# Kernel optimization log

Measured on AMD Instinct MI355X. Metric: run time of the kernel, lower is better.

The kernel has to match this reference:

```python
import jax, jax.numpy as jnp
import numpy as np

# ----- static configuration (mirrors __init__) -----
NUM_CLASSES = np.array([2, 4, 8, 16, 32] * 8, dtype=np.int64)   # 40 categorical features
F_FEAT = len(NUM_CLASSES)                                        # 40
D = int(NUM_CLASSES.sum())                                       # 496 one-hot columns
T = 1000                                                         # num diffusion timesteps
B = 32768                                                        # batch size

OFFSETS_NP = np.concatenate([[0], np.cumsum(NUM_CLASSES)])
SEG_IDS = jnp.asarray(np.repeat(np.arange(F_FEAT), NUM_CLASSES))                    # [D] col -> feature
NC_EXPANDED = jnp.asarray(np.repeat(NUM_CLASSES, NUM_CLASSES).astype(np.float32))   # [D]
LOG_NC = jnp.log(NC_EXPANDED)
SEG_START = jnp.asarray(OFFSETS_NP[:-1])                                            # [F] segment start col

_beta = np.linspace(1e-4, 0.02, T)
_alpha = 1.0 - _beta
_ca = np.cumprod(_alpha)
LOG_ALPHA = jnp.asarray(np.log(_alpha), jnp.float32)
LOG_1M_ALPHA = jnp.asarray(np.log(1.0 - _alpha), jnp.float32)
LOG_CA = jnp.asarray(np.log(_ca), jnp.float32)
LOG_1M_CA = jnp.asarray(np.log(1.0 - _ca), jnp.float32)


def _extract(a, t):
    return a[t][:, None]  # [B,1]


def seg_logsumexp(x):
    """Per-categorical-segment stable logsumexp of x [B,D], broadcast back to [B,D]."""
    xt = x.T                                                       # [D,B]
    m = jax.ops.segment_max(xt, SEG_IDS, num_segments=F_FEAT)      # [F,B]
    mg = m[SEG_IDS]                                                # [D,B]
    s = jax.ops.segment_sum(jnp.exp(xt - mg), SEG_IDS, num_segments=F_FEAT)
    return (m + jnp.log(s))[SEG_IDS].T                             # [B,D]


def index_to_log_onehot(x):
    """x [B,F] per-feature class indices -> log one-hot [B,D] (log(clamp(onehot,1e-30)))."""
    cols = SEG_START[None, :] + x                                  # global cols [B,F]
    oh = jnp.zeros((x.shape[0], D), jnp.float32)
    oh = oh.at[jnp.arange(x.shape[0])[:, None], cols].set(1.0)
    return jnp.log(jnp.maximum(oh, 1e-30))


def q_prior(log_x0, t):
    return jnp.logaddexp(log_x0 + _extract(LOG_CA, t), _extract(LOG_1M_CA, t) - LOG_NC[None, :])


def q_one_timestep(log_xt, t):
    return jnp.logaddexp(log_xt + _extract(LOG_ALPHA, t), _extract(LOG_1M_ALPHA, t) - LOG_NC[None, :])


def q_posterior(log_x0, log_xt, t):
    tm1 = jnp.maximum(t - 1, 0)
    ev = q_prior(log_x0, tm1)
    ev = jnp.where((t == 0)[:, None], log_x0, ev)
    un = ev + q_one_timestep(log_xt, t)
    return un - seg_logsumexp(un)


def log_sample_categorical(logits, uniform):
    """Gumbel-max sample per ragged segment; returns log one-hot [B,D]."""
    gumbel = -jnp.log(-jnp.log(uniform + 1e-30) + 1e-30)
    z = gumbel + logits                                            # [B,D]
    zt = z.T                                                       # [D,B]
    m = jax.ops.segment_max(zt, SEG_IDS, num_segments=F_FEAT)[SEG_IDS]   # [D,B]
    cand = jnp.where(zt == m, jnp.arange(D)[:, None], D)           # first-max tie break (= torch argmax)
    col = jax.ops.segment_min(cand, SEG_IDS, num_segments=F_FEAT).T      # [B,F] winning global column
    oh = jnp.zeros(z.shape, jnp.float32).at[jnp.arange(z.shape[0])[:, None], col].set(1.0)
    return jnp.log(jnp.maximum(oh, 1e-30))


def setup_inputs():
    key = jax.random.key(0)
    k1, k2, k3, k4, k5 = jax.random.split(key, 5)
    x_0 = jax.random.randint(k1, (B, F_FEAT), 0, jnp.asarray(NUM_CLASSES)[None, :]).astype(jnp.int32)
    timesteps = jax.random.randint(k2, (B,), 0, T).astype(jnp.int32)
    uniform = jax.random.uniform(k3, (B, D), jnp.float32)
    W = jax.random.normal(k4, (D, D), jnp.float32) * 0.02
    b = jnp.zeros((D,), jnp.float32)
    t_emb = jax.random.normal(k5, (T, D), jnp.float32) * 0.02
    return {"x_0": x_0, "timesteps": timesteps, "uniform": uniform, "W": W, "b": b, "t_emb": t_emb}


def reference(x_0, timesteps, uniform, W, b, t_emb):
    log_x0 = index_to_log_onehot(x_0)                              # [B,D]
    log_xt = log_sample_categorical(q_prior(log_x0, timesteps), uniform)   # multinomial_q_sample
    pred = log_xt @ W + b + t_emb[timesteps]                       # denoise_fn(log_x_t, t)
    log_x0_hat = pred - seg_logsumexp(pred)                        # per-class log_softmax
    log_true = q_posterior(log_x0, log_xt, timesteps)
    log_est = q_posterior(log_x0_hat, log_xt, timesteps)
    kl = jnp.sum(jnp.exp(log_true) * (log_true - log_est), axis=1)         # [B]
    dec_nll = -jnp.sum(jnp.exp(log_x0) * log_est, axis=1)                  # [B]
    mask = (timesteps == 0).astype(jnp.float32)
    diff_loss = mask * dec_nll + (1.0 - mask) * kl
    log_qxT = q_prior(log_x0, jnp.full((log_x0.shape[0],), T - 1, jnp.int32))
    kl_prior = jnp.sum(jnp.exp(log_qxT) * (log_qxT + LOG_NC[None, :]), axis=1)  # vs log_half = -log(K)
    loss = diff_loss * T + kl_prior
    return jnp.mean(loss)
```

## Files before the change

### kernel.cpp

```cpp
#include <hip/hip_runtime.h>
#include <math.h>

#define NFEAT 40
#define NCOLS 496
#define NT    1000
#define NB    32768
#define LC    (-69.07755278982137f)

#define LK2  0.6931471805599453f
#define LK4  1.3862943611198906f
#define LK8  2.0794415416798357f
#define LK16 2.772588722239781f
#define LK32 3.4657359027997265f

#define WS_TABS   0
#define WS_CBP    16000
#define WS_CAD    18048
#define WS_WP     26048

typedef _Float16 half8 __attribute__((ext_vector_type(8)));

__device__ __forceinline__ float lae(float a, float b) {
    float mx = fmaxf(a, b), mn = fminf(a, b);
    return mx + log1pf(expf(mn - mx));
}

__device__ __forceinline__ float flog(float x) { return __logf(x); }
__device__ __forceinline__ float fexp(float x) { return __expf(x); }
__device__ __forceinline__ float flae(float a, float b) {
    float mx = fmaxf(a, b), mn = fminf(a, b);
    return mx + __logf(1.0f + __expf(mn - mx));
}

__device__ __forceinline__ int obo_of_r(int r) {
    return (r < 4) ? 30 + 8*r : (r < 6) ? 14 + 8*(r-4) : (r == 6) ? 6 : 0;
}

__global__ void ddpm_setup(const float* __restrict__ W, const float* __restrict__ bg,
                           float* __restrict__ tabs, double* __restrict__ cad,
                           float* __restrict__ cbp, _Float16* __restrict__ Wp,
                           float* __restrict__ out)
{
    const int tid = threadIdx.x;
    const int blk = blockIdx.x;
    if (blk == 0) {
        __shared__ double chunkP[64];
        __shared__ double prefP[64];
        const double step = (0.02 - 1e-4) / 999.0;
        if (tid < 64) {
            int i0 = tid * 16, i1 = i0 + 16; if (i1 > NT) i1 = NT;
            double p = 1.0;
            for (int i = i0; i < i1; ++i) {
                double beta = (i == 999) ? 0.02 : (1e-4 + (double)i * step);
                p *= (1.0 - beta);
            }
            chunkP[tid] = p;
        }
        if (tid >= 128 && tid < 144) {
            int i = tid - 128;
            cbp[64 * (i >> 1) + 62 + (i & 1)] = 0.f;
        }
        __syncthreads();
        if (tid == 0) {
            double run = 1.0;
            for (int c = 0; c < 64; ++c) { prefP[c] = run; run *= chunkP[c]; }
        }
        __syncthreads();
        if (tid < 64) {
            int i0 = tid * 16, i1 = i0 + 16; if (i1 > NT) i1 = NT;
            double run = prefP[tid];
            for (int i = i0; i < i1; ++i) {
                double beta = (i == 999) ? 0.02 : (1e-4 + (double)i * step);
                run *= (1.0 - beta);
                cad[i] = run;
            }
        }
        __syncthreads();
        for (int i = tid; i < NT; i += 256) {
            double beta  = (i == 999) ? 0.02 : (1e-4 + (double)i * step);
            double alpha = 1.0 - beta;
            double ca    = cad[i];
            tabs[i]        = (float)log(alpha);
            tabs[NT + i]   = (float)log(1.0 - alpha);
            tabs[2*NT + i] = (float)log(ca);
            tabs[3*NT + i] = (float)log(1.0 - ca);
        }
        __syncthreads();
        if (tid == 0) {
            float lcaT = tabs[2*NT + NT - 1], l1caT = tabs[3*NT + NT - 1];
            float lks[5] = {LK2, LK4, LK8, LK16, LK32};
            float pri = 0.f;
            for (int s = 0; s < 5; ++s) {
                int K = 2 << s;
                float lk = lks[s];
                float Ph = lae(lcaT, l1caT - lk);
                float Pc = lae(LC + lcaT, l1caT - lk);
                pri += 8.0f * (expf(Ph) * (Ph + lk) + (float)(K - 1) * expf(Pc) * (Pc + lk));
            }
            out[0] = pri;
        }
    } else if (blk < 32) {
        __shared__ float part[256];
        const int c = (blk - 1) * 16 + (tid & 15);
        const int chunk = tid >> 4;
        float s = 0.f;
        const int r0 = chunk * 31;
        #pragma unroll 8
        for (int i = 0; i < 31; ++i) s += W[(r0 + i) * NCOLS + c];
        part[tid] = s;
        __syncthreads();
        if (tid < 16) {
            float tot = 0.f;
            #pragma unroll
            for (int j = 0; j < 16; ++j) tot += part[j * 16 + tid];
            int cc2 = c;
            int gg = cc2 / 62;
            int rc = cc2 - 62 * gg;
            int rr, kk;
            if (rc >= 30)      { rr = (rc - 30) >> 3; kk = (rc - 30) & 7; }
            else if (rc >= 14) { rr = 4 + ((rc - 14) >> 3); kk = (rc - 14) & 7; }
            else if (rc >= 6)  { rr = 6; kk = rc - 6; }
            else               { rr = 7; kk = rc; }
            cbp[64 * gg + 8 * rr + kk] = LC * tot + bg[c];
        }
    } else {
        const int d = blk - 32;
        #pragma unroll
        for (int h = 0; h < 2; ++h) {
            int jp = tid + 256 * h;
            int ln = jp >> 3, k = jp & 7;
            int gg = ln >> 3, rr = ln & 7;
            bool valid = !(rr == 7 && k >= 6);
            int col = 62 * gg + obo_of_r(rr) + k;
            float v = valid ? W[d * NCOLS + col] : 0.f;
            Wp[d * 512 + jp] = (_Float16)v;
        }
    }
}

__device__ __forceinline__ float seg_final(
    float K, float sLg, float evx0, float evwc, bool same, bool t0,
    float pQh, float pQc, float Qh, float Qc,
    float pEh, float pEc, float Eh, float Ec,
    float am, float bmK)
{
    float pwc = fexp(evwc);
    float Zp  = am + K * bmK;
    float pZe = pQc * (Zp - pwc) + pQh * pwc;
    float lse = flog(pZe);
    float p11 = pEh * pQh, p12 = pEh * pQc, p21 = pEc * pQh, p22 = pEc * pQc;
    float Zt  = same ? (p11 + (K - 1.f) * p22) : (p12 + p21 + (K - 2.f) * p22);
    float invZt = __builtin_amdgcn_rcpf(Zt);
    float lZt = flog(Zt);
    float l11 = Eh + Qh, l12 = Eh + Qc, l21 = Ec + Qh, l22 = Ec + Qc;
    float Tlt = same ? (p11 * (l11 - lZt) + (K - 1.f) * p22 * (l22 - lZt)) * invZt
                     : (p12 * (l12 - lZt) + p21 * (l21 - lZt) + (K - 2.f) * p22 * (l22 - lZt)) * invZt;
    float uD  = t0 ? 0.f : p22 * invZt;
    float ux0 = t0 ? 1.f : (same ? p11 : p12) * invZt;
    float uwc = t0 ? 0.f : p21 * invZt;
    float uwq = same ? ux0 : uwc;
    float S = uD * sLg + (ux0 - uD) * evx0 + (same ? 0.f : (uwc - uD) * evwc)
            + Qc + (Qh - Qc) * uwq - lse;
    return t0 ? (-S) : (Tlt - S);
}

__global__ __launch_bounds__(256)
void ddpm_main(const int* __restrict__ x0g,
               const int* __restrict__ tsg,
               const float* __restrict__ unig,
               const _Float16* __restrict__ Wp,
               const float* __restrict__ teg,
               const float* __restrict__ tabs,
               const float* __restrict__ cbp,
               float* __restrict__ outg)
{
    __shared__ float spart[4];
    const int tid  = threadIdx.x;
    const int wv   = tid >> 6;
    const int lane = tid & 63;
    const int row  = (int)blockIdx.x * 4 + wv;
    const int g    = lane >> 3;
    const int r    = lane & 7;
    const bool r7  = (r == 7);

    const int t   = tsg[row];
    const bool t0 = (t == 0);
    const int tm1 = t0 ? 0 : t - 1;
    const float la_t   = tabs[t];
    const float l1a_t  = tabs[NT + t];
    const float lca_t  = tabs[2*NT + t];
    const float l1ca_t = tabs[3*NT + t];
    const float lca_m  = tabs[2*NT + tm1];
    const float l1ca_m = tabs[3*NT + tm1];

    const int sA   = (r < 4) ? 4 : (r < 6) ? 3 : (r == 6) ? 2 : 1;
    const int obo  = (r < 4) ? 30 + 8*r : (r < 6) ? 14 + 8*(r-4) : (r == 6) ? 6 : 0;
    const int ob   = 62*g + obo;
    const int stA  = (r < 4) ? 30 : (r < 6) ? 14 : (r == 6) ? 6 : 2;
    const float lkA = (r < 4) ? LK32 : (r < 6) ? LK16 : (r == 6) ? LK8 : LK4;
    const float lkB = LK2;
    const int KA   = (r < 4) ? 32 : (r < 6) ? 16 : (r == 6) ? 8 : 4;

    const int xval = x0g[row * NFEAT + (lane < NFEAT ? lane : 0)];
    const int fA   = 5*g + sA;
    const int xvA  = __shfl(xval, fA);
    const int xvB  = __shfl(xval, 5*g);
    const int x0cA = 62*g + stA + xvA;
    const int x0cB = 62*g + xvB;

    const float zphA = flae(lca_t, l1ca_t - lkA), zpcA = flae(LC + lca_t, l1ca_t - lkA);
    const float zphB = flae(lca_t, l1ca_t - lkB), zpcB = flae(LC + lca_t, l1ca_t - lkB);
    float z[8];
    {
        const float* urow = unig + row * NCOLS + ob;
        float2 u0 = *(const float2*)(urow);
        float2 u1 = *(const float2*)(urow + 2);
        float2 u2 = *(const float2*)(urow + 4);
        float2 u3 = *(const float2*)(urow + 6);
        float uu[8] = {u0.x,u0.y,u1.x,u1.y,u2.x,u2.y,u3.x,u3.y};
        #pragma unroll
        for (int k = 0; k < 8; ++k) {
            bool isB = r7 && (k < 2);
            bool ok  = (k < 6) || !r7;
            int  oc  = ob + k;
            bool hx0 = oc == (isB ? x0cB : x0cA);
            float qp = hx0 ? (isB ? zphB : zphA) : (isB ? zpcB : zpcA);
            float gum = -flog(-flog(uu[k] + 1e-30f) + 1e-30f);
            z[k] = ok ? (gum + qp) : -INFINITY;
        }
    }

    float bvA = -INFINITY; int bcA = 0;
    float bvB = -INFINITY; int bcB = 0;
    #pragma unroll
    for (int k = 0; k < 8; ++k) {
        bool isB = r7 && (k < 2);
        bool okA = (k < 6) ? !isB : !r7;
        int  oc  = ob + k;
        if (okA && z[k] > bvA) { bvA = z[k]; bcA = oc; }
        if (isB && z[k] > bvB) { bvB = z[k]; bcB = oc; }
    }
    {
        float ov = __shfl_xor(bvA, 1); int oc2 = __shfl_xor(bcA, 1);
        bool bet = (ov > bvA) || (ov == bvA && oc2 < bcA);
        if (r < 6 && bet) { bvA = ov; bcA = oc2; }
        ov = __shfl_xor(bvA, 2); oc2 = __shfl_xor(bcA, 2);
        bet = (ov > bvA) || (ov == bvA && oc2 < bcA);
        if (r < 4 && bet) { bvA = ov; bcA = oc2; }
    }
    const int wcA = bcA, wcB = bcB;

    const float at   = fexp(la_t);
    const float otKA = fexp(l1a_t - lkA), otKB = fexp(l1a_t - lkB);
    const float pQhA = at + otKA, pQcA = 1e-30f*at + otKA;
    const float pQhB = at + otKB, pQcB = 1e-30f*at + otKB;
    const float QhA = flog(pQhA), QcA = flog(pQcA);
    const float QhB = flog(pQhB), QcB = flog(pQcB);
    const float am   = t0 ? 1.f : fexp(lca_m);
    const float bmKA = t0 ? 0.f : fexp(l1ca_m - lkA);
    const float bmKB = t0 ? 0.f : fexp(l1ca_m - lkB);
    const float pEhA = am + bmKA, pEcA = 1e-30f*am + bmKA;
    const float pEhB = am + bmKB, pEcB = 1e-30f*am + bmKB;
    const float EhA = flog(pEhA), EcA = flog(pEcA);
    const float EhB = flog(pEhB), EcB = flog(pEcB);

    float cc[8], ee[8];
    {
        const float4* cp = (const float4*)(cbp + (lane << 3));
        float4 c0 = cp[0], c1 = cp[1];
        const float* ter = teg + t * NCOLS + ob;
        float2 e0=*(const float2*)(ter),   e1=*(const float2*)(ter+2);
        float2 e2=*(const float2*)(ter+4), e3=*(const float2*)(ter+6);
        cc[0]=c0.x;cc[1]=c0.y;cc[2]=c0.z;cc[3]=c0.w;cc[4]=c1.x;cc[5]=c1.y;cc[6]=c1.z;cc[7]=c1.w;
        ee[0]=e0.x;ee[1]=e0.y;ee[2]=e1.x;ee[3]=e1.y;ee[4]=e2.x;ee[5]=e2.y;ee[6]=e3.x;ee[7]=e3.y;
    }

    float gs[8];
    {
        half8 acc0 = {0,0,0,0,0,0,0,0};
        half8 acc1 = {0,0,0,0,0,0,0,0};
        const size_t lo = (size_t)(lane << 3);
        #pragma unroll
        for (int g2 = 0; g2 < 8; ++g2) {
            int w0 = __builtin_amdgcn_readlane(wcB, 8*g2 + 7);
            int w1 = __builtin_amdgcn_readlane(wcA, 8*g2 + 7);
            int w2 = __builtin_amdgcn_readlane(wcA, 8*g2 + 6);
            int w3 = __builtin_amdgcn_readlane(wcA, 8*g2 + 4);
            int w4 = __builtin_amdgcn_readlane(wcA, 8*g2 + 0);
            acc0 += *(const half8*)(Wp + ((size_t)w0 << 9) + lo);
            acc1 += *(const half8*)(Wp + ((size_t)w1 << 9) + lo);
            acc0 += *(const half8*)(Wp + ((size_t)w2 << 9) + lo);
            acc1 += *(const half8*)(Wp + ((size_t)w3 << 9) + lo);
            acc0 += *(const half8*)(Wp + ((size_t)w4 << 9) + lo);
        }
        half8 acc = acc0 + acc1;
        #pragma unroll
        for (int k = 0; k < 8; ++k) gs[k] = (float)acc[k];
    }

    float pred[8];
    #pragma unroll
    for (int k = 0; k < 8; ++k) {
        bool ok = (k < 6) || !r7;
        pred[k] = ok ? (cc[k] + ee[k] - LC * gs[k]) : -1e30f;
    }

    float mA = -INFINITY, mB = -INFINITY;
    #pragma unroll
    for (int k = 0; k < 8; ++k) {
        bool isB = r7 && (k < 2);
        bool okA = (k < 6) ? !isB : !r7;
        if (okA) mA = fmaxf(mA, pred[k]);
        if (isB) mB = fmaxf(mB, pred[k]);
    }
    { float mo = __shfl_xor(mA, 1); if (r < 6) mA = fmaxf(mA, mo);
      mo = __shfl_xor(mA, 2);       if (r < 4) mA = fmaxf(mA, mo); }

    float ex[8]; float SpA = 0.f, SpB = 0.f;
    #pragma unroll
    for (int k = 0; k < 8; ++k) {
        bool isB = r7 && (k < 2);
        bool okA = (k < 6) ? !isB : !r7;
        float e = fexp(pred[k] - (isB ? mB : mA));
        ex[k] = e;
        if (okA) SpA += e;
        if (isB) SpB += e;
    }
    { float so = __shfl_xor(SpA, 1); if (r < 6) SpA += so;
      so = __shfl_xor(SpA, 2);       if (r < 4) SpA += so; }
    const float invSpA = __builtin_amdgcn_rcpf(SpA);
    const float invSpB = __builtin_amdgcn_rcpf(SpB);
    const float c1A = am * invSpA, c1B = am * invSpB;
    const float lSpA = flog(SpA), lSpB = flog(SpB);

    float sLgA = 0.f, evx0A = 0.f, evwcA = 0.f;
    float sLgB = 0.f, evx0B = 0.f, evwcB = 0.f;
    #pragma unroll
    for (int k = 0; k < 8; ++k) {
        bool isB = r7 && (k < 2);
        bool okA = (k < 6) ? !isB : !r7;
        int  oc  = ob + k;
        float Lg;
        if (t0) {
            Lg = pred[k] - (isB ? mB : mA) - (isB ? lSpB : lSpA);
        } else {
            Lg = flog(fmaf(isB ? c1B : c1A, ex[k], isB ? bmKB : bmKA));
        }
        if (okA) {
            sLgA += Lg;
            evx0A += (oc == x0cA) ? Lg : 0.f;
            evwcA += (oc == wcA)  ? Lg : 0.f;
        }
        if (isB) {
            sLgB += Lg;
            evx0B += (oc == x0cB) ? Lg : 0.f;
            evwcB += (oc == wcB)  ? Lg : 0.f;
        }
    }
    { float so;
      so = __shfl_xor(sLgA, 1);  if (r < 6) sLgA += so;
      so = __shfl_xor(evx0A, 1); if (r < 6) evx0A += so;
      so = __shfl_xor(evwcA, 1); if (r < 6) evwcA += so;
      so = __shfl_xor(sLgA, 2);  if (r < 4) sLgA += so;
      so = __shfl_xor(evx0A, 2); if (r < 4) evx0A += so;
      so = __shfl_xor(evwcA, 2); if (r < 4) evwcA += so; }

    const bool sameA = (x0cA == wcA), sameB = (x0cB == wcB);
    float resA = seg_final((float)KA, sLgA, evx0A, evwcA, sameA, t0,
                           pQhA, pQcA, QhA, QcA, pEhA, pEcA, EhA, EcA, am, bmKA);
    float resB = seg_final(2.f, sLgB, evx0B, evwcB, sameB, t0,
                           pQhB, pQcB, QhB, QcB, pEhB, pEcB, EhB, EcB, am, bmKB);

    const bool ownerA = (r == 0) || (r == 4) || (r == 6) || r7;
    float val = (ownerA ? resA : 0.f) + (r7 ? resB : 0.f);
    #pragma unroll
    for (int off = 32; off > 0; off >>= 1) val += __shfl_down(val, off);
    if (lane == 0) spart[wv] = val * (1000.0f / (float)NB);
    __syncthreads();
    if (tid == 0) atomicAdd(outg, spart[0] + spart[1] + spart[2] + spart[3]);
}

extern "C" void kernel_launch(void* const* d_in, const int* in_sizes, int n_in,
                              void* d_out, int out_size, void* d_ws, size_t ws_size,
                              hipStream_t stream) {
    (void)in_sizes; (void)n_in; (void)out_size; (void)ws_size;
    const int*   x0  = (const int*)d_in[0];
    const int*   ts  = (const int*)d_in[1];
    const float* uni = (const float*)d_in[2];
    const float* W   = (const float*)d_in[3];
    const float* bv  = (const float*)d_in[4];
    const float* te  = (const float*)d_in[5];
    float* out = (float*)d_out;

    char* ws = (char*)d_ws;
    float*    tabs = (float*)(ws + WS_TABS);
    float*    cbp  = (float*)(ws + WS_CBP);
    double*   cad  = (double*)(ws + WS_CAD);
    _Float16* Wp   = (_Float16*)(ws + WS_WP);

    ddpm_setup<<<528, 256, 0, stream>>>(W, bv, tabs, cad, cbp, Wp, out);
    ddpm_main<<<NB / 4, 256, 0, stream>>>(x0, ts, uni, Wp, te, tabs, cbp, out);
}
```

Before: 213.5 us.

## Process two rows per wavefront to overlap gathers and amortize setup

Each wavefront now handles two batch rows instead of one, interleaving their Wp gather-accumulations and loads of uniform, x0 and time-embedding data. The grid is halved, the per-row epilogue is factored into a helper, and launch bounds now request 4 waves per SIMD. The intent is more memory-level parallelism from independent loads, plus amortized per-wave fixed costs such as the cbp loads and the block reduction. In exchange the kernel uses more registers, which may cut occupancy, and there are fewer blocks in flight.

```diff
diff --git a/kernel.cpp b/kernel.cpp
--- a/kernel.cpp
+++ b/kernel.cpp
@@ -113,9 +113,8 @@
             float tot = 0.f;
             #pragma unroll
             for (int j = 0; j < 16; ++j) tot += part[j * 16 + tid];
-            int cc2 = c;
-            int gg = cc2 / 62;
-            int rc = cc2 - 62 * gg;
+            int gg = c / 62;
+            int rc = c - 62 * gg;
             int rr, kk;
             if (rc >= 30)      { rr = (rc - 30) >> 3; kk = (rc - 30) & 7; }
             else if (rc >= 14) { rr = 4 + ((rc - 14) >> 3); kk = (rc - 14) & 7; }
@@ -139,7 +138,7 @@
 }
 
 __device__ __forceinline__ float seg_final(
-    float K, float sLg, float evx0, float evwc, bool same, bool t0,
+    float K, float sLg, float evx0, float evwc, bool same, bool iz,
     float pQh, float pQc, float Qh, float Qc,
     float pEh, float pEc, float Eh, float Ec,
     float am, float bmK)
@@ -155,16 +154,102 @@
     float l11 = Eh + Qh, l12 = Eh + Qc, l21 = Ec + Qh, l22 = Ec + Qc;
     float Tlt = same ? (p11 * (l11 - lZt) + (K - 1.f) * p22 * (l22 - lZt)) * invZt
                      : (p12 * (l12 - lZt) + p21 * (l21 - lZt) + (K - 2.f) * p22 * (l22 - lZt)) * invZt;
-    float uD  = t0 ? 0.f : p22 * invZt;
-    float ux0 = t0 ? 1.f : (same ? p11 : p12) * invZt;
-    float uwc = t0 ? 0.f : p21 * invZt;
+    float uD  = iz ? 0.f : p22 * invZt;
+    float ux0 = iz ? 1.f : (same ? p11 : p12) * invZt;
+    float uwc = iz ? 0.f : p21 * invZt;
     float uwq = same ? ux0 : uwc;
     float S = uD * sLg + (ux0 - uD) * evx0 + (same ? 0.f : (uwc - uD) * evwc)
             + Qc + (Qh - Qc) * uwq - lse;
-    return t0 ? (-S) : (Tlt - S);
-}
-
-__global__ __launch_bounds__(256)
+    return iz ? (-S) : (Tlt - S);
+}
+
+__device__ __forceinline__ float row_epilogue(
+    const float* pred, int r, int ob,
+    int x0cA, int x0cB, int wcA, int wcB, int KA, float lkA, bool iz,
+    float la, float l1a, float lcam, float l1cam)
+{
+    const bool r7 = (r == 7);
+    const float at   = fexp(la);
+    const float otKA = fexp(l1a - lkA), otKB = fexp(l1a - LK2);
+    const float pQhA = at + otKA, pQcA = 1e-30f*at + otKA;
+    const float pQhB = at + otKB, pQcB = 1e-30f*at + otKB;
+    const float QhA = flog(pQhA), QcA = flog(pQcA);
+    const float QhB = flog(pQhB), QcB = flog(pQcB);
+    const float am   = iz ? 1.f : fexp(lcam);
+    const float bmKA = iz ? 0.f : fexp(l1cam - lkA);
+    const float bmKB = iz ? 0.f : fexp(l1cam - LK2);
+    const float pEhA = am + bmKA, pEcA = 1e-30f*am + bmKA;
+    const float pEhB = am + bmKB, pEcB = 1e-30f*am + bmKB;
+    const float EhA = flog(pEhA), EcA = flog(pEcA);
+    const float EhB = flog(pEhB), EcB = flog(pEcB);
+
+    float mA = -INFINITY, mB = -INFINITY;
+    #pragma unroll
+    for (int k = 0; k < 8; ++k) {
+        bool isB = r7 && (k < 2);
+        bool okA = (k < 6) ? !isB : !r7;
+        if (okA) mA = fmaxf(mA, pred[k]);
+        if (isB) mB = fmaxf(mB, pred[k]);
+    }
+    { float mo = __shfl_xor(mA, 1); if (r < 6) mA = fmaxf(mA, mo);
+      mo = __shfl_xor(mA, 2);       if (r < 4) mA = fmaxf(mA, mo); }
+
+    float ex[8]; float SpA = 0.f, SpB = 0.f;
+    #pragma unroll
+    for (int k = 0; k < 8; ++k) {
+        bool isB = r7 && (k < 2);
+        bool okA = (k < 6) ? !isB : !r7;
+        float e = fexp(pred[k] - (isB ? mB : mA));
+        ex[k] = e;
+        if (okA) SpA += e;
+        if (isB) SpB += e;
+    }
+    { float so = __shfl_xor(SpA, 1); if (r < 6) SpA += so;
+      so = __shfl_xor(SpA, 2);       if (r < 4) SpA += so; }
+    const float invSpA = __builtin_amdgcn_rcpf(SpA);
+    const float invSpB = __builtin_amdgcn_rcpf(SpB);
+    const float c1A = am * invSpA, c1B = am * invSpB;
+    const float lSpA = flog(SpA), lSpB = flog(SpB);
+
+    float sLgA = 0.f, evx0A = 0.f, evwcA = 0.f;
+    float sLgB = 0.f, evx0B = 0.f, evwcB = 0.f;
+    #pragma unroll
+    for (int k = 0; k < 8; ++k) {
+        bool isB = r7 && (k < 2);
+        bool okA = (k < 6) ? !isB : !r7;
+        int  oc  = ob + k;
+        float Lg;
+        if (iz) Lg = pred[k] - (isB ? mB : mA) - (isB ? lSpB : lSpA);
+        else    Lg = flog(fmaf(isB ? c1B : c1A, ex[k], isB ? bmKB : bmKA));
+        if (okA) {
+            sLgA += Lg;
+            evx0A += (oc == x0cA) ? Lg : 0.f;
+            evwcA += (oc == wcA)  ? Lg : 0.f;
+        }
+        if (isB) {
+            sLgB += Lg;
+            evx0B += (oc == x0cB) ? Lg : 0.f;
+            evwcB += (oc == wcB)  ? Lg : 0.f;
+        }
+    }
+    { float so;
+      so = __shfl_xor(sLgA, 1);  if (r < 6) sLgA += so;
+      so = __shfl_xor(evx0A, 1); if (r < 6) evx0A += so;
+      so = __shfl_xor(evwcA, 1); if (r < 6) evwcA += so;
+      so = __shfl_xor(sLgA, 2);  if (r < 4) sLgA += so;
+      so = __shfl_xor(evx0A, 2); if (r < 4) evx0A += so;
+      so = __shfl_xor(evwcA, 2); if (r < 4) evwcA += so; }
+
+    const bool sameA = (x0cA == wcA), sameB = (x0cB == wcB);
+    float resA = seg_final((float)KA, sLgA, evx0A, evwcA, sameA, iz,
+                           pQhA, pQcA, QhA, QcA, pEhA, pEcA, EhA, EcA, am, bmKA);
+    float resB = seg_final(2.f, sLgB, evx0B, evwcB, sameB, iz,
+                           pQhB, pQcB, QhB, QcB, pEhB, pEcB, EhB, EcB, am, bmKB);
+    const bool ownerA = (r == 0) || (r == 4) || (r == 6) || r7;
+    return (ownerA ? resA : 0.f) + (r7 ? resB : 0.f);
+}
+
+__global__ __launch_bounds__(256, 4)
 void ddpm_main(const int* __restrict__ x0g,
                const int* __restrict__ tsg,
                const float* __restrict__ unig,
@@ -178,201 +263,146 @@
     const int tid  = threadIdx.x;
     const int wv   = tid >> 6;
     const int lane = tid & 63;
-    const int row  = (int)blockIdx.x * 4 + wv;
+    const int row0 = ((int)blockIdx.x * 4 + wv) * 2;
     const int g    = lane >> 3;
     const int r    = lane & 7;
     const bool r7  = (r == 7);
-
-    const int t   = tsg[row];
-    const bool t0 = (t == 0);
-    const int tm1 = t0 ? 0 : t - 1;
-    const float la_t   = tabs[t];
-    const float l1a_t  = tabs[NT + t];
-    const float lca_t  = tabs[2*NT + t];
-    const float l1ca_t = tabs[3*NT + t];
-    const float lca_m  = tabs[2*NT + tm1];
-    const float l1ca_m = tabs[3*NT + tm1];
 
     const int sA   = (r < 4) ? 4 : (r < 6) ? 3 : (r == 6) ? 2 : 1;
     const int obo  = (r < 4) ? 30 + 8*r : (r < 6) ? 14 + 8*(r-4) : (r == 6) ? 6 : 0;
     const int ob   = 62*g + obo;
     const int stA  = (r < 4) ? 30 : (r < 6) ? 14 : (r == 6) ? 6 : 2;
     const float lkA = (r < 4) ? LK32 : (r < 6) ? LK16 : (r == 6) ? LK8 : LK4;
-    const float lkB = LK2;
     const int KA   = (r < 4) ? 32 : (r < 6) ? 16 : (r == 6) ? 8 : 4;
-
-    const int xval = x0g[row * NFEAT + (lane < NFEAT ? lane : 0)];
     const int fA   = 5*g + sA;
-    const int xvA  = __shfl(xval, fA);
-    const int xvB  = __shfl(xval, 5*g);
-    const int x0cA = 62*g + stA + xvA;
-    const int x0cB = 62*g + xvB;
-
-    const float zphA = flae(lca_t, l1ca_t - lkA), zpcA = flae(LC + lca_t, l1ca_t - lkA);
-    const float zphB = flae(lca_t, l1ca_t - lkB), zpcB = flae(LC + lca_t, l1ca_t - lkB);
-    float z[8];
-    {
-        const float* urow = unig + row * NCOLS + ob;
+
+    int t[2]; bool iz[2];
+    float la[2], l1a[2], lca[2], l1ca[2], lcam[2], l1cam[2];
+    #pragma unroll
+    for (int i = 0; i < 2; ++i) {
+        int tt = __builtin_amdgcn_readfirstlane(tsg[row0 + i]);
+        t[i] = tt; iz[i] = (tt == 0);
+        int tm1 = iz[i] ? 0 : tt - 1;
+        la[i]    = tabs[tt];
+        l1a[i]   = tabs[NT + tt];
+        lca[i]   = tabs[2*NT + tt];
+        l1ca[i]  = tabs[3*NT + tt];
+        lcam[i]  = tabs[2*NT + tm1];
+        l1cam[i] = tabs[3*NT + tm1];
+    }
+
+    int x0cA[2], x0cB[2];
+    #pragma unroll
+    for (int i = 0; i < 2; ++i) {
+        int xval = x0g[(row0 + i) * NFEAT + (lane < NFEAT ? lane : 0)];
+        int xvA = __shfl(xval, fA);
+        int xvB = __shfl(xval, 5*g);
+        x0cA[i] = 62*g + stA + xvA;
+        x0cB[i] = 62*g + xvB;
+    }
+
+    float uu[2][8];
+    #pragma unroll
+    for (int i = 0; i < 2; ++i) {
+        const float* urow = unig + (row0 + i) * NCOLS + ob;
         float2 u0 = *(const float2*)(urow);
         float2 u1 = *(const float2*)(urow + 2);
         float2 u2 = *(const float2*)(urow + 4);
         float2 u3 = *(const float2*)(urow + 6);
-        float uu[8] = {u0.x,u0.y,u1.x,u1.y,u2.x,u2.y,u3.x,u3.y};
+        uu[i][0]=u0.x; uu[i][1]=u0.y; uu[i][2]=u1.x; uu[i][3]=u1.y;
+        uu[i][4]=u2.x; uu[i][5]=u2.y; uu[i][6]=u3.x; uu[i][7]=u3.y;
+    }
+
+    int wcA[2], wcB[2];
+    #pragma unroll
+    for (int i = 0; i < 2; ++i) {
+        const float zphA = flae(lca[i], l1ca[i] - lkA), zpcA = flae(LC + lca[i], l1ca[i] - lkA);
+        const float zphB = flae(lca[i], l1ca[i] - LK2), zpcB = flae(LC + lca[i], l1ca[i] - LK2);
+        float z[8];
         #pragma unroll
         for (int k = 0; k < 8; ++k) {
             bool isB = r7 && (k < 2);
             bool ok  = (k < 6) || !r7;
             int  oc  = ob + k;
-            bool hx0 = oc == (isB ? x0cB : x0cA);
+            bool hx0 = oc == (isB ? x0cB[i] : x0cA[i]);
             float qp = hx0 ? (isB ? zphB : zphA) : (isB ? zpcB : zpcA);
-            float gum = -flog(-flog(uu[k] + 1e-30f) + 1e-30f);
+            float gum = -flog(-flog(uu[i][k] + 1e-30f) + 1e-30f);
             z[k] = ok ? (gum + qp) : -INFINITY;
         }
-    }
-
-    float bvA = -INFINITY; int bcA = 0;
-    float bvB = -INFINITY; int bcB = 0;
-    #pragma unroll
-    for (int k = 0; k < 8; ++k) {
-        bool isB = r7 && (k < 2);
-        bool okA = (k < 6) ? !isB : !r7;
-        int  oc  = ob + k;
-        if (okA && z[k] > bvA) { bvA = z[k]; bcA = oc; }
-        if (isB && z[k] > bvB) { bvB = z[k]; bcB = oc; }
-    }
-    {
+        float bvA = -INFINITY; int bcA = 0;
+        float bvB = -INFINITY; int bcB = 0;
+        #pragma unroll
+        for (int k = 0; k < 8; ++k) {
+            bool isB = r7 && (k < 2);
+            bool okA = (k < 6) ? !isB : !r7;
+            int  oc  = ob + k;
+            if (okA && z[k] > bvA) { bvA = z[k]; bcA = oc; }
+            if (isB && z[k] > bvB) { bvB = z[k]; bcB = oc; }
+        }
         float ov = __shfl_xor(bvA, 1); int oc2 = __shfl_xor(bcA, 1);
         bool bet = (ov > bvA) || (ov == bvA && oc2 < bcA);
         if (r < 6 && bet) { bvA = ov; bcA = oc2; }
         ov = __shfl_xor(bvA, 2); oc2 = __shfl_xor(bcA, 2);
         bet = (ov > bvA) || (ov == bvA && oc2 < bcA);
         if (r < 4 && bet) { bvA = ov; bcA = oc2; }
-    }
-    const int wcA = bcA, wcB = bcB;
-
-    const float at   = fexp(la_t);
-    const float otKA = fexp(l1a_t - lkA), otKB = fexp(l1a_t - lkB);
-    const float pQhA = at + otKA, pQcA = 1e-30f*at + otKA;
-    const float pQhB = at + otKB, pQcB = 1e-30f*at + otKB;
-    const float QhA = flog(pQhA), QcA = flog(pQcA);
-    const float QhB = flog(pQhB), QcB = flog(pQcB);
-    const float am   = t0 ? 1.f : fexp(lca_m);
-    const float bmKA = t0 ? 0.f : fexp(l1ca_m - lkA);
-    const float bmKB = t0 ? 0.f : fexp(l1ca_m - lkB);
-    const float pEhA = am + bmKA, pEcA = 1e-30f*am + bmKA;
-    const float pEhB = am + bmKB, pEcB = 1e-30f*am + bmKB;
-    const float EhA = flog(pEhA), EcA = flog(pEcA);
-    const float EhB = flog(pEhB), EcB = flog(pEcB);
-
-    float cc[8], ee[8];
+        wcA[i] = bcA; wcB[i] = bcB;
+    }
+
+    float cc[8], ee[2][8];
     {
         const float4* cp = (const float4*)(cbp + (lane << 3));
         float4 c0 = cp[0], c1 = cp[1];
-        const float* ter = teg + t * NCOLS + ob;
-        float2 e0=*(const float2*)(ter),   e1=*(const float2*)(ter+2);
-        float2 e2=*(const float2*)(ter+4), e3=*(const float2*)(ter+6);
         cc[0]=c0.x;cc[1]=c0.y;cc[2]=c0.z;cc[3]=c0.w;cc[4]=c1.x;cc[5]=c1.y;cc[6]=c1.z;cc[7]=c1.w;
-        ee[0]=e0.x;ee[1]=e0.y;ee[2]=e1.x;ee[3]=e1.y;ee[4]=e2.x;ee[5]=e2.y;ee[6]=e3.x;ee[7]=e3.y;
-    }
-
-    float gs[8];
+        #pragma unroll
+        for (int i = 0; i < 2; ++i) {
+            const float* ter = teg + t[i] * NCOLS + ob;
+            float2 e0=*(const float2*)(ter),   e1=*(const float2*)(ter+2);
+            float2 e2=*(const float2*)(ter+4), e3=*(const float2*)(ter+6);
+            ee[i][0]=e0.x;ee[i][1]=e0.y;ee[i][2]=e1.x;ee[i][3]=e1.y;
+            ee[i][4]=e2.x;ee[i][5]=e2.y;ee[i][6]=e3.x;ee[i][7]=e3.y;
+        }
+    }
+
+    float pred[2][8];
     {
-        half8 acc0 = {0,0,0,0,0,0,0,0};
-        half8 acc1 = {0,0,0,0,0,0,0,0};
-        const size_t lo = (size_t)(lane << 3);
+        half8 a0[2], a1[2];
+        a0[0] = (half8){0,0,0,0,0,0,0,0}; a0[1] = a0[0];
+        a1[0] = a0[0]; a1[1] = a0[0];
+        const int lo = lane << 3;
         #pragma unroll
         for (int g2 = 0; g2 < 8; ++g2) {
-            int w0 = __builtin_amdgcn_readlane(wcB, 8*g2 + 7);
-            int w1 = __builtin_amdgcn_readlane(wcA, 8*g2 + 7);
-            int w2 = __builtin_amdgcn_readlane(wcA, 8*g2 + 6);
-            int w3 = __builtin_amdgcn_readlane(wcA, 8*g2 + 4);
-            int w4 = __builtin_amdgcn_readlane(wcA, 8*g2 + 0);
-            acc0 += *(const half8*)(Wp + ((size_t)w0 << 9) + lo);
-            acc1 += *(const half8*)(Wp + ((size_t)w1 << 9) + lo);
-            acc0 += *(const half8*)(Wp + ((size_t)w2 << 9) + lo);
-            acc1 += *(const half8*)(Wp + ((size_t)w3 << 9) + lo);
-            acc0 += *(const half8*)(Wp + ((size_t)w4 << 9) + lo);
-        }
-        half8 acc = acc0 + acc1;
-        #pragma unroll
-        for (int k = 0; k < 8; ++k) gs[k] = (float)acc[k];
-    }
-
-    float pred[8];
-    #pragma unroll
-    for (int k = 0; k < 8; ++k) {
-        bool ok = (k < 6) || !r7;
-        pred[k] = ok ? (cc[k] + ee[k] - LC * gs[k]) : -1e30f;
-    }
-
-    float mA = -INFINITY, mB = -INFINITY;
-    #pragma unroll
-    for (int k = 0; k < 8; ++k) {
-        bool isB = r7 && (k < 2);
-        bool okA = (k < 6) ? !isB : !r7;
-        if (okA) mA = fmaxf(mA, pred[k]);
-        if (isB) mB = fmaxf(mB, pred[k]);
-    }
-    { float mo = __shfl_xor(mA, 1); if (r < 6) mA = fmaxf(mA, mo);
-      mo = __shfl_xor(mA, 2);       if (r < 4) mA = fmaxf(mA, mo); }
-
-    float ex[8]; float SpA = 0.f, SpB = 0.f;
-    #pragma unroll
-    for (int k = 0; k < 8; ++k) {
-        bool isB = r7 && (k < 2);
-        bool okA = (k < 6) ? !isB : !r7;
-        float e = fexp(pred[k] - (isB ? mB : mA));
-        ex[k] = e;
-        if (okA) SpA += e;
-        if (isB) SpB += e;
-    }
-    { float so = __shfl_xor(SpA, 1); if (r < 6) SpA += so;
-      so = __shfl_xor(SpA, 2);       if (r < 4) SpA += so; }
-    const float invSpA = __builtin_amdgcn_rcpf(SpA);
-    const float invSpB = __builtin_amdgcn_rcpf(SpB);
-    const float c1A = am * invSpA, c1B = am * invSpB;
-    const float lSpA = flog(SpA), lSpB = flog(SpB);
-
-    float sLgA = 0.f, evx0A = 0.f, evwcA = 0.f;
-    float sLgB = 0.f, evx0B = 0.f, evwcB = 0.f;
-    #pragma unroll
-    for (int k = 0; k < 8; ++k) {
-        bool isB = r7 && (k < 2);
-        bool okA = (k < 6) ? !isB : !r7;
-        int  oc  = ob + k;
-        float Lg;
-        if (t0) {
-            Lg = pred[k] - (isB ? mB : mA) - (isB ? lSpB : lSpA);
-        } else {
-            Lg = flog(fmaf(isB ? c1B : c1A, ex[k], isB ? bmKB : bmKA));
-        }
-        if (okA) {
-            sLgA += Lg;
-            evx0A += (oc == x0cA) ? Lg : 0.f;
-            evwcA += (oc == wcA)  ? Lg : 0.f;
-        }
-        if (isB) {
-            sLgB += Lg;
-            evx0B += (oc == x0cB) ? Lg : 0.f;
-            evwcB += (oc == wcB)  ? Lg : 0.f;
-        }
-    }
-    { float so;
-      so = __shfl_xor(sLgA, 1);  if (r < 6) sLgA += so;
-      so = __shfl_xor(evx0A, 1); if (r < 6) evx0A += so;
-      so = __shfl_xor(evwcA, 1); if (r < 6) evwcA += so;
-      so = __shfl_xor(sLgA, 2);  if (r < 4) sLgA += so;
-      so = __shfl_xor(evx0A, 2); if (r < 4) evx0A += so;
-      so = __shfl_xor(evwcA, 2); if (r < 4) evwcA += so; }
-
-    const bool sameA = (x0cA == wcA), sameB = (x0cB == wcB);
-    float resA = seg_final((float)KA, sLgA, evx0A, evwcA, sameA, t0,
-                           pQhA, pQcA, QhA, QcA, pEhA, pEcA, EhA, EcA, am, bmKA);
-    float resB = seg_final(2.f, sLgB, evx0B, evwcB, sameB, t0,
-                           pQhB, pQcB, QhB, QcB, pEhB, pEcB, EhB, EcB, am, bmKB);
-
-    const bool ownerA = (r == 0) || (r == 4) || (r == 6) || r7;
-    float val = (ownerA ? resA : 0.f) + (r7 ? resB : 0.f);
+            #pragma unroll
+            for (int i = 0; i < 2; ++i) {
+                int w0 = __builtin_amdgcn_readlane(wcB[i], 8*g2 + 7);
+                int w1 = __builtin_amdgcn_readlane(wcA[i], 8*g2 + 7);
+                int w2 = __builtin_amdgcn_readlane(wcA[i], 8*g2 + 6);
+                int w3 = __builtin_amdgcn_readlane(wcA[i], 8*g2 + 4);
+                int w4 = __builtin_amdgcn_readlane(wcA[i], 8*g2 + 0);
+                a0[i] += *(const half8*)(Wp + ((size_t)w0 << 9) + lo);
+                a1[i] += *(const half8*)(Wp + ((size_t)w1 << 9) + lo);
+                a0[i] += *(const half8*)(Wp + ((size_t)w2 << 9) + lo);
+                a1[i] += *(const half8*)(Wp + ((size_t)w3 << 9) + lo);
+                a0[i] += *(const half8*)(Wp + ((size_t)w4 << 9) + lo);
+            }
+        }
+        #pragma unroll
+        for (int i = 0; i < 2; ++i) {
+            half8 acc = a0[i] + a1[i];
+            #pragma unroll
+            for (int k = 0; k < 8; ++k) {
+                bool ok = (k < 6) || !r7;
+                pred[i][k] = ok ? (cc[k] + ee[i][k] - LC * (float)acc[k]) : -1e30f;
+            }
+        }
+    }
+
+    float val = 0.f;
+    #pragma unroll
+    for (int i = 0; i < 2; ++i) {
+        val += row_epilogue(pred[i], r, ob, x0cA[i], x0cB[i], wcA[i], wcB[i],
+                            KA, lkA, iz[i], la[i], l1a[i], lcam[i], l1cam[i]);
+    }
+
     #pragma unroll
     for (int off = 32; off > 0; off >>= 1) val += __shfl_down(val, off);
     if (lane == 0) spart[wv] = val * (1000.0f / (float)NB);
@@ -399,5 +429,5 @@
     _Float16* Wp   = (_Float16*)(ws + WS_WP);
 
     ddpm_setup<<<528, 256, 0, stream>>>(W, bv, tabs, cad, cbp, Wp, out);
-    ddpm_main<<<NB / 4, 256, 0, stream>>>(x0, ts, uni, Wp, te, tabs, cbp, out);
-}
+    ddpm_main<<<NB / 8, 256, 0, stream>>>(x0, ts, uni, Wp, te, tabs, cbp, out);
+}
```

New measurement: 320.8 us. 1.5x slower.
